# Kernel tuning notes

Hardware: AMD Instinct MI355X
Metric: run time of the kernel (lower is better)

The kernel has to match this reference:

```python
import jax, jax.numpy as jnp
import numpy as np

TEMP = 1.0
PRIOR = 0.2
THRESHOLD = 0.5
EPS = 1.1920929e-07  # torch float32 eps used by probs_to_logits / clamp_probs


def setup_inputs() -> dict:
    key = jax.random.key(0)
    k1, k2, k3, k4, k5 = jax.random.split(key, 5)
    B, L, D = 8, 8192, 256
    hidden = jax.random.normal(k1, (B, L, D), dtype=jnp.float32)
    # q/k projections are initialized to identity in the module; perturb slightly
    Wq = jnp.eye(D, dtype=jnp.float32) + 0.02 * jax.random.normal(k2, (D, D), dtype=jnp.float32)
    Wk = jnp.eye(D, dtype=jnp.float32) + 0.02 * jax.random.normal(k3, (D, D), dtype=jnp.float32)
    # uniform noise for the RelaxedBernoulli reparameterized sample
    noise = jax.random.uniform(k4, (B, L), dtype=jnp.float32)
    # ragged lengths -> contiguous attention mask (1s then 0s), as the module assumes
    lengths = jax.random.randint(k5, (B,), L // 2, L + 1)
    attention_mask = (jnp.arange(L)[None, :] < lengths[:, None]).astype(jnp.float32)
    return {"hidden": hidden, "Wq": Wq, "Wk": Wk, "noise": noise, "attention_mask": attention_mask}


def _binomial_loss(k, n, p):
    # -log Binomial(n, p).log_prob(k) / n
    logp = (jax.scipy.special.gammaln(n + 1.0)
            - jax.scipy.special.gammaln(k + 1.0)
            - jax.scipy.special.gammaln(n - k + 1.0)
            + k * jnp.log(p) + (n - k) * jnp.log1p(-p))
    return -logp / n


def reference(hidden, Wq, Wk, noise, attention_mask):
    B, L, D = hidden.shape
    # F.normalize along last dim (eps=1e-12), then linear projections (no bias)
    hn = hidden / jnp.maximum(jnp.linalg.norm(hidden, axis=-1, keepdims=True), 1e-12)
    q = jnp.einsum('bld,ed->ble', hn[:, :-1], Wq)
    k = jnp.einsum('bld,ed->ble', hn[:, 1:], Wk)
    cos_sim = jnp.sum(q * k, axis=-1)                      # [B, L-1]
    probs = jnp.clip((1.0 - cos_sim) * 0.5, 0.0, 1.0)
    probs = jnp.pad(probs, ((0, 0), (1, 0)), constant_values=1.0)  # boundary forced at t=0

    # RelaxedBernoulli(temp, probs).rsample() with externally supplied uniforms
    p = jnp.clip(probs, EPS, 1.0 - EPS)
    logits = jnp.log(p) - jnp.log1p(-p)
    u = jnp.clip(noise, EPS, 1.0 - EPS)
    soft = jax.nn.sigmoid((logits + jnp.log(u) - jnp.log1p(-u)) / TEMP)
    hard = (soft > THRESHOLD).astype(soft.dtype)
    hard = jax.lax.stop_gradient(hard - soft) + soft       # straight-through

    # mask out boundaries in padding; force a boundary at the last real token
    hard = hard * attention_mask
    pad_mask = attention_mask == 0
    first_pad = pad_mask & (jnp.cumsum(pad_mask.astype(jnp.int32), axis=1) == 1)
    last_real = jnp.roll(first_pad, shift=-1, axis=1).at[:, -1].set(False)
    hard = jnp.maximum(hard, last_real.astype(hard.dtype))

    # downsample: mean-pool tokens within each boundary-delimited segment.
    # boundary==1 starts a new segment; segment id = cumsum(hard) - 1.
    hard_bin = jax.lax.stop_gradient(hard) > 0.5
    seg = jnp.cumsum(hard_bin.astype(jnp.int32), axis=1) - 1
    seg = jnp.clip(seg, 0, L - 1)
    flat_seg = (seg + jnp.arange(B, dtype=jnp.int32)[:, None] * L).reshape(-1)  # [B*L]
    w = attention_mask.reshape(-1)                                              # pads excluded
    sums = jax.ops.segment_sum(hidden.reshape(-1, D) * w[:, None], flat_seg, num_segments=B * L)
    cnts = jax.ops.segment_sum(w, flat_seg, num_segments=B * L)
    pooled = (sums / (cnts + 1e-9)[:, None]).reshape(B, L, D)  # [B, S_max<=L, D], zero-padded

    n_b = jnp.sum(hard, axis=1)                  # boundaries per batch row
    num_boundaries = jnp.sum(n_b)
    total_positions = jnp.sum(attention_mask)
    # gathered mask values at kept positions are all 1 -> prefix-ones of length n_b
    shortened_attention_mask = (jnp.arange(L)[None, :]
                                < jax.lax.stop_gradient(n_b)[:, None]).astype(jnp.float32)
    loss = _binomial_loss(num_boundaries, total_positions, PRIOR)
    return pooled, loss, num_boundaries, total_positions, shortened_attention_mask
```

## Files before the change

kernel.cpp:

```cpp
#include <hip/hip_runtime.h>
#include <hip/hip_bf16.h>
#include <math.h>

#define L_SEQ 8192
#define B_BATCH 8
#define D_DIM 256
#define BL (B_BATCH * L_SEQ)
#define EPS_F 1.1920929e-07f

typedef __attribute__((ext_vector_type(8))) short short8;
typedef __attribute__((ext_vector_type(4))) float f32x4;
typedef __attribute__((ext_vector_type(4))) unsigned short u16x4;


__device__ inline unsigned short f2bf(float x) {
    __hip_bfloat16 b = __float2bfloat16(x);
    return *(unsigned short*)&b;
}
__device__ inline float bf2f(unsigned short u) {
    __hip_bfloat16 b = *(__hip_bfloat16*)&u;
    return __bfloat162float(b);
}

__global__ __launch_bounds__(256) void k_matMpack(
    const float* __restrict__ Wq, const float* __restrict__ Wk,
    unsigned short* __restrict__ Bpack) {
    __shared__ float Aq[64][33];
    __shared__ float Ak[64][17];
    const int f   = blockIdx.x;
    const int k8  = f >> 4, ct = f & 15;
    const int tid = threadIdx.x;
    const int n   = tid & 15;
    const int k   = tid >> 4;
    float a0 = 0.f, a1 = 0.f;
    for (int e0 = 0; e0 < 256; e0 += 64) {
        for (int i = tid; i < 64 * 32; i += 256) {
            const int e = i >> 5, d = i & 31;
            Aq[e][d] = Wq[(e0 + e) * 256 + k8 * 32 + d];
        }
        for (int i = tid; i < 64 * 16; i += 256) {
            const int e = i >> 4, d = i & 15;
            Ak[e][d] = Wk[(e0 + e) * 256 + ct * 16 + d];
        }
        __syncthreads();
#pragma unroll 8
        for (int e = 0; e < 64; ++e) {
            a0 += Aq[e][k] * Ak[e][n];
            a1 += Aq[e][k + 16] * Ak[e][n];
        }
        __syncthreads();
    }
    const int col = ct * 16 + n;
    const float M0 = a0 - ((k8 * 32 + k)      == col ? 1.0f : 0.0f);
    const float M1 = a1 - ((k8 * 32 + k + 16) == col ? 1.0f : 0.0f);
    const unsigned short h0 = f2bf(M0), h1 = f2bf(M1);
    const unsigned short l0 = f2bf(M0 - bf2f(h0)), l1 = f2bf(M1 - bf2f(h1));
    unsigned short* dstH = Bpack + (size_t)(k8 * 16 + ct) * 512;
    unsigned short* dstL = dstH + 128 * 512;
    const int q0 = k >> 3, j0 = k & 7;
    const int q1 = (k + 16) >> 3;
    dstH[(q0 * 16 + n) * 8 + j0] = h0;
    dstH[(q1 * 16 + n) * 8 + j0] = h1;
    dstL[(q0 * 16 + n) * 8 + j0] = l0;
    dstL[(q1 * 16 + n) * 8 + j0] = l1;
}

#define RS 264
#define MM(A,Bv,C) __builtin_amdgcn_mfma_f32_16x16x32_bf16((A),(Bv),(C),0,0,0)
#define MFMA8(V0,V1,BN) \
    acc[0][0]=MM(V0,BN##_0,acc[0][0]); acc[0][1]=MM(V0,BN##_1,acc[0][1]); \
    acc[0][2]=MM(V0,BN##_2,acc[0][2]); acc[0][3]=MM(V0,BN##_3,acc[0][3]); \
    acc[1][0]=MM(V1,BN##_0,acc[1][0]); acc[1][1]=MM(V1,BN##_1,acc[1][1]); \
    acc[1][2]=MM(V1,BN##_2,acc[1][2]); acc[1][3]=MM(V1,BN##_3,acc[1][3]);
#define LOADB(BN,S) \
    BN##_0 = Bld[(((S) * 16) + wc4 + 0) * 64]; \
    BN##_1 = Bld[(((S) * 16) + wc4 + 1) * 64]; \
    BN##_2 = Bld[(((S) * 16) + wc4 + 2) * 64]; \
    BN##_3 = Bld[(((S) * 16) + wc4 + 3) * 64];
#define STRIP_HL(S,BN) { \
    const int co = ((S) & 7) * 32; \
    const short8 hv0 = *(const short8*)(hA0 + co), hv1 = *(const short8*)(hA1 + co); \
    const short8 lv0 = *(const short8*)(lA0 + co), lv1 = *(const short8*)(lA1 + co); \
    MFMA8(hv0, hv1, BN); \
    MFMA8(lv0, lv1, BN); \
    LOADB(BN, (S) + 3); }
#define STRIP_H(S,BN) { \
    const int co = ((S) & 7) * 32; \
    const short8 hv0 = *(const short8*)(hA0 + co), hv1 = *(const short8*)(hA1 + co); \
    MFMA8(hv0, hv1, BN); \
    if ((S) + 3 < 16) { LOADB(BN, (S) + 3); } }

__global__ __launch_bounds__(512, 4) void k_cosmfma(
    const float* __restrict__ hidden, const unsigned short* __restrict__ Bpack,
    const float* __restrict__ noise, unsigned char* __restrict__ hard) {
    __shared__ __attribute__((aligned(16))) unsigned short hiA[65 * RS];
    __shared__ __attribute__((aligned(16))) unsigned short loA[65 * RS];
    __shared__ float Vpart[4][64];
    __shared__ float dots[64];

    const int tid  = threadIdx.x;
    const int lane = tid & 63;
    const int w    = tid >> 6;
    const int wr   = w >> 2;
    const int wc   = w & 3;
    const int wr32 = wr * 32;
    const int wc4  = wc * 4;
    const int T0   = blockIdx.x * 64;

    const short8* __restrict__ Bld = (const short8*)Bpack + lane;

    short8 bA_0, bA_1, bA_2, bA_3, bB_0, bB_1, bB_2, bB_3, bC_0, bC_1, bC_2, bC_3;
    LOADB(bA, 0);
    LOADB(bB, 1);
    LOADB(bC, 2);

    {
        const int r0 = w * 8;
        int tokA = T0 - 1 + r0; if (tokA < 0) tokA = 0;
        float4 vb0 = ((const float4*)hidden)[(size_t)tokA * 64 + lane];
        float4 vb1 = ((const float4*)hidden)[(size_t)(T0 + r0) * 64 + lane];
        float4 hp4 = {0.f, 0.f, 0.f, 0.f};
#pragma unroll 1
        for (int ii = 0; ii <= 8; ++ii) {
            const float4 vcur = vb0;
            vb0 = vb1;
            if (ii + 2 <= 8)
                vb1 = ((const float4*)hidden)[(size_t)(T0 + r0 + ii + 1) * 64 + lane];
            float ss = vcur.x * vcur.x + vcur.y * vcur.y + vcur.z * vcur.z + vcur.w * vcur.w;
#pragma unroll
            for (int sh = 32; sh >= 1; sh >>= 1) ss += __shfl_xor(ss, sh);
            const float inv = 1.0f / fmaxf(sqrtf(ss), 1e-12f);
            float4 h4;
            h4.x = vcur.x * inv; h4.y = vcur.y * inv;
            h4.z = vcur.z * inv; h4.w = vcur.w * inv;
            const unsigned short hx = f2bf(h4.x), hy = f2bf(h4.y),
                                 hz = f2bf(h4.z), hw2 = f2bf(h4.w);
            const u16x4 hv4 = {hx, hy, hz, hw2};
            const u16x4 lv4 = {f2bf(h4.x - bf2f(hx)), f2bf(h4.y - bf2f(hy)),
                               f2bf(h4.z - bf2f(hz)), f2bf(h4.w - bf2f(hw2))};
            const int i = r0 + ii;
            *(u16x4*)&hiA[i * RS + lane * 4] = hv4;
            *(u16x4*)&loA[i * RS + lane * 4] = lv4;
            if (ii > 0) {
                float pd = h4.x * hp4.x + h4.y * hp4.y + h4.z * hp4.z + h4.w * hp4.w;
#pragma unroll
                for (int sh = 32; sh >= 1; sh >>= 1) pd += __shfl_xor(pd, sh);
                if (lane == 0) dots[i - 1] = pd;
            }
            hp4 = h4;
        }
    }
    __syncthreads();

    const int m = lane & 15, q = lane >> 4;
    const unsigned short* __restrict__ hA0 = &hiA[(wr32 +  0 + m) * RS + q * 8];
    const unsigned short* __restrict__ hA1 = &hiA[(wr32 + 16 + m) * RS + q * 8];
    const unsigned short* __restrict__ lA0 = &loA[(wr32 +  0 + m) * RS + q * 8];
    const unsigned short* __restrict__ lA1 = &loA[(wr32 + 16 + m) * RS + q * 8];

    f32x4 acc[2][4];
#pragma unroll
    for (int af = 0; af < 2; ++af)
#pragma unroll
        for (int c = 0; c < 4; ++c) { f32x4 z = {0.f, 0.f, 0.f, 0.f}; acc[af][c] = z; }

    STRIP_HL(0, bA)  STRIP_HL(1, bB)  STRIP_HL(2, bC)  STRIP_HL(3, bA)
    STRIP_HL(4, bB)  STRIP_HL(5, bC)  STRIP_HL(6, bA)  STRIP_HL(7, bB)
    STRIP_H (8, bC)  STRIP_H (9, bA)  STRIP_H (10, bB) STRIP_H (11, bC)
    STRIP_H (12, bA) STRIP_H (13, bB) STRIP_H (14, bC) STRIP_H (15, bA)

#pragma unroll
    for (int af = 0; af < 2; ++af) {
#pragma unroll
        for (int r = 0; r < 4; ++r) {
            const int row = wr32 + af * 16 + (q << 2) + r;
            const int ib  = (row + 1) * RS + wc4 * 16 + m;
            float pp = acc[af][0][r] * (bf2f(hiA[ib     ]) + bf2f(loA[ib     ]))
                     + acc[af][1][r] * (bf2f(hiA[ib + 16]) + bf2f(loA[ib + 16]))
                     + acc[af][2][r] * (bf2f(hiA[ib + 32]) + bf2f(loA[ib + 32]))
                     + acc[af][3][r] * (bf2f(hiA[ib + 48]) + bf2f(loA[ib + 48]));
            pp += __shfl_xor(pp, 1);
            pp += __shfl_xor(pp, 2);
            pp += __shfl_xor(pp, 4);
            pp += __shfl_xor(pp, 8);
            if (m == 0) Vpart[wc][row] = pp;
        }
    }
    __syncthreads();
    if (tid < 64) {
        const int rl = tid;
        const float part = Vpart[0][rl] + Vpart[1][rl] + Vpart[2][rl] + Vpart[3][rl];
        const int t = T0 + rl;
        const int l = t & (L_SEQ - 1);
        float p;
        if (l == 0) {
            p = 1.0f;
        } else {
            p = (1.0f - (part + dots[rl])) * 0.5f;
            p = fminf(fmaxf(p, 0.0f), 1.0f);
        }
        p = fminf(fmaxf(p, EPS_F), 1.0f - EPS_F);
        float u = noise[t];
        u = fminf(fmaxf(u, EPS_F), 1.0f - EPS_F);
        const float z = ((logf(p) - log1pf(-p)) + logf(u)) - log1pf(-u);
        hard[t] = (z > 0.0f) ? (unsigned char)1 : (unsigned char)0;
    }
}

__global__ __launch_bounds__(1024) void k_scan(
    const float* __restrict__ mask, const unsigned char* __restrict__ hard,
    int* __restrict__ starts, int* __restrict__ nb_arr,
    int* __restrict__ len_arr, float* __restrict__ out_short) {
    __shared__ int wsum[16];
    __shared__ int s_len;
    const int b = blockIdx.x, tid = threadIdx.x;
    const int lane = tid & 63, wv = tid >> 6;
    const int base = b * L_SEQ;

    const float4* m4 = (const float4*)(mask + base);
    const float4 va = m4[tid * 2], vb = m4[tid * 2 + 1];
    int cnt = (va.x != 0.f) + (va.y != 0.f) + (va.z != 0.f) + (va.w != 0.f)
            + (vb.x != 0.f) + (vb.y != 0.f) + (vb.z != 0.f) + (vb.w != 0.f);
#pragma unroll
    for (int sh = 32; sh >= 1; sh >>= 1) cnt += __shfl_xor(cnt, sh);
    if (lane == 0) wsum[wv] = cnt;
    __syncthreads();
    if (tid == 0) {
        int s = 0;
        for (int i = 0; i < 16; ++i) s += wsum[i];
        s_len = s;
    }
    __syncthreads();
    const int len = s_len;

    const int i0 = tid * 8;
    const uint2 hb = ((const uint2*)(hard + base))[tid];
    int c = 0;
    unsigned int bits = 0;
#pragma unroll
    for (int j = 0; j < 8; ++j) {
        const unsigned int byte = ((j < 4 ? hb.x : hb.y) >> (8 * (j & 3))) & 0xffu;
        int h = ((i0 + j) < len) ? (int)(byte != 0u) : 0;
        if (len < L_SEQ && (i0 + j) == len - 1) h = 1;
        bits |= (unsigned int)h << j;
        c += h;
    }
    int x = c;
#pragma unroll
    for (int ofs = 1; ofs < 64; ofs <<= 1) {
        const int t = __shfl_up(x, ofs);
        if (lane >= ofs) x += t;
    }
    if (lane == 63) wsum[wv] = x;
    __syncthreads();
    int woff = 0, nb = 0;
#pragma unroll
    for (int i = 0; i < 16; ++i) {
        const int t = wsum[i];
        nb += t;
        if (i < wv) woff += t;
    }
    int run = woff + x - c;
#pragma unroll
    for (int j = 0; j < 8; ++j)
        if ((bits >> j) & 1u) { starts[base + run] = i0 + j; ++run; }

    if (tid == 0) { nb_arr[b] = nb; len_arr[b] = len; }

    float4 o0, o1;
    o0.x = (i0 + 0) < nb ? 1.f : 0.f; o0.y = (i0 + 1) < nb ? 1.f : 0.f;
    o0.z = (i0 + 2) < nb ? 1.f : 0.f; o0.w = (i0 + 3) < nb ? 1.f : 0.f;
    o1.x = (i0 + 4) < nb ? 1.f : 0.f; o1.y = (i0 + 5) < nb ? 1.f : 0.f;
    o1.z = (i0 + 6) < nb ? 1.f : 0.f; o1.w = (i0 + 7) < nb ? 1.f : 0.f;
    float4* os4 = (float4*)(out_short + base);
    os4[tid * 2] = o0;
    os4[tid * 2 + 1] = o1;
}

__global__ __launch_bounds__(256) void k_pool(
    const float* __restrict__ hidden, const int* __restrict__ starts,
    const int* __restrict__ nb_arr, const int* __restrict__ len_arr,
    float* __restrict__ pooled) {
    const int tid  = threadIdx.x;
    const int lane = tid & 63;
    const int wid  = blockIdx.x * 4 + (tid >> 6);
    const int b    = wid >> 13;
    const int s    = wid & (L_SEQ - 1);
    const int nb   = nb_arr[b];

    float4 res = {0.f, 0.f, 0.f, 0.f};
    if (s < nb) {
        const int start = (s == 0) ? 0 : starts[b * L_SEQ + s];
        const int end   = (s + 1 < nb) ? starts[b * L_SEQ + s + 1] : len_arr[b];
        float4 acc = {0.f, 0.f, 0.f, 0.f};
        for (int t = start; t < end; ++t) {
            const float4 v = ((const float4*)hidden)[(b * L_SEQ + t) * 64 + lane];
            acc.x += v.x; acc.y += v.y; acc.z += v.z; acc.w += v.w;
        }
        const float cntf = (float)(end - start);
        res.x = acc.x / cntf; res.y = acc.y / cntf; res.z = acc.z / cntf; res.w = acc.w / cntf;
    }
    ((float4*)pooled)[(size_t)wid * 64 + lane] = res;
}

__global__ void k_final(const int* __restrict__ nb_arr, const int* __restrict__ len_arr,
                        float* __restrict__ out_scal) {
    if (threadIdx.x == 0) {
        int nb = 0, ln = 0;
        for (int b = 0; b < B_BATCH; ++b) { nb += nb_arr[b]; ln += len_arr[b]; }
        const double k = (double)nb, n = (double)ln;
        const double logp = lgamma(n + 1.0) - lgamma(k + 1.0) - lgamma(n - k + 1.0)
                            + k * log(0.2) + (n - k) * log(0.8);
        const double loss = -logp / n;
        out_scal[0] = (float)loss;
        out_scal[1] = (float)nb;
        out_scal[2] = (float)ln;
    }
}

extern "C" void kernel_launch(void* const* d_in, const int* in_sizes, int n_in,
                              void* d_out, int out_size, void* d_ws, size_t ws_size,
                              hipStream_t stream) {
    const float* hidden = (const float*)d_in[0];
    const float* Wq     = (const float*)d_in[1];
    const float* Wk     = (const float*)d_in[2];
    const float* noise  = (const float*)d_in[3];
    const float* mask   = (const float*)d_in[4];
    float* out = (float*)d_out;
    char* ws = (char*)d_ws;

    int*            starts = (int*)(ws);
    unsigned short* Bpack  = (unsigned short*)(ws + 262144);
    unsigned char*  hard   = (unsigned char*)(ws + 524288);
    int*            nb_arr = (int*)(ws + 589824);
    int*            len_arr= (int*)(ws + 589856);

    float* pooled = out;
    float* scal   = out + (size_t)BL * D_DIM;
    float* shortm = scal + 3;

    k_matMpack<<<128, 256, 0, stream>>>(Wq, Wk, Bpack);
    k_cosmfma <<<BL / 64, 512, 0, stream>>>(hidden, Bpack, noise, hard);
    k_scan    <<<B_BATCH, 1024, 0, stream>>>(mask, hard, starts, nb_arr, len_arr, shortm);
    k_pool    <<<BL / 4, 256, 0, stream>>>(hidden, starts, nb_arr, len_arr, pooled);
    k_final   <<<1, 64, 0, stream>>>(nb_arr, len_arr, scal);
}
```

Before: 180.6 us.

## Split MFMA K-dimension across wave pairs instead of splitting rows

Changes the wave decomposition of the cosine-similarity MFMA from splitting the 64 rows across two wave groups to splitting the K dimension in half. Each wave now covers all 64 rows with 4x4 accumulators, and the partial results are reduced across 8 Vpart slots. Each wave now loads only half of the B matrix fragments, which cuts global B traffic and register prefetch depth. In exchange it doubles accumulator registers and adds a larger final reduction, and the occupancy hint moves to an amdgpu_waves_per_eu attribute.

```diff
diff --git a/kernel.cpp b/kernel.cpp
--- a/kernel.cpp
+++ b/kernel.cpp
@@ -67,52 +67,59 @@
 
 #define RS 264
 #define MM(A,Bv,C) __builtin_amdgcn_mfma_f32_16x16x32_bf16((A),(Bv),(C),0,0,0)
-#define MFMA8(V0,V1,BN) \
+#define MFMA16(V0,V1,V2,V3,BN) \
     acc[0][0]=MM(V0,BN##_0,acc[0][0]); acc[0][1]=MM(V0,BN##_1,acc[0][1]); \
     acc[0][2]=MM(V0,BN##_2,acc[0][2]); acc[0][3]=MM(V0,BN##_3,acc[0][3]); \
     acc[1][0]=MM(V1,BN##_0,acc[1][0]); acc[1][1]=MM(V1,BN##_1,acc[1][1]); \
-    acc[1][2]=MM(V1,BN##_2,acc[1][2]); acc[1][3]=MM(V1,BN##_3,acc[1][3]);
-#define LOADB(BN,S) \
-    BN##_0 = Bld[(((S) * 16) + wc4 + 0) * 64]; \
-    BN##_1 = Bld[(((S) * 16) + wc4 + 1) * 64]; \
-    BN##_2 = Bld[(((S) * 16) + wc4 + 2) * 64]; \
-    BN##_3 = Bld[(((S) * 16) + wc4 + 3) * 64];
-#define STRIP_HL(S,BN) { \
-    const int co = ((S) & 7) * 32; \
-    const short8 hv0 = *(const short8*)(hA0 + co), hv1 = *(const short8*)(hA1 + co); \
-    const short8 lv0 = *(const short8*)(lA0 + co), lv1 = *(const short8*)(lA1 + co); \
-    MFMA8(hv0, hv1, BN); \
-    MFMA8(lv0, lv1, BN); \
-    LOADB(BN, (S) + 3); }
-#define STRIP_H(S,BN) { \
-    const int co = ((S) & 7) * 32; \
-    const short8 hv0 = *(const short8*)(hA0 + co), hv1 = *(const short8*)(hA1 + co); \
-    MFMA8(hv0, hv1, BN); \
-    if ((S) + 3 < 16) { LOADB(BN, (S) + 3); } }
-
-__global__ __launch_bounds__(512, 4) void k_cosmfma(
+    acc[1][2]=MM(V1,BN##_2,acc[1][2]); acc[1][3]=MM(V1,BN##_3,acc[1][3]); \
+    acc[2][0]=MM(V2,BN##_0,acc[2][0]); acc[2][1]=MM(V2,BN##_1,acc[2][1]); \
+    acc[2][2]=MM(V2,BN##_2,acc[2][2]); acc[2][3]=MM(V2,BN##_3,acc[2][3]); \
+    acc[3][0]=MM(V3,BN##_0,acc[3][0]); acc[3][1]=MM(V3,BN##_1,acc[3][1]); \
+    acc[3][2]=MM(V3,BN##_2,acc[3][2]); acc[3][3]=MM(V3,BN##_3,acc[3][3]);
+#define LOADB(BN,J) { \
+    BN##_0 = Bw[(((J) < 4 ? (J) : (J) + 4) * 16 + 0) * 64]; \
+    BN##_1 = Bw[(((J) < 4 ? (J) : (J) + 4) * 16 + 1) * 64]; \
+    BN##_2 = Bw[(((J) < 4 ? (J) : (J) + 4) * 16 + 2) * 64]; \
+    BN##_3 = Bw[(((J) < 4 ? (J) : (J) + 4) * 16 + 3) * 64]; }
+#define COMP_HL(J,BN) { \
+    const short8 hv0 = *(const short8*)(hbase2 + ( 0*16)*RS + ((J)&3)*32); \
+    const short8 hv1 = *(const short8*)(hbase2 + ( 1*16)*RS + ((J)&3)*32); \
+    const short8 hv2 = *(const short8*)(hbase2 + ( 2*16)*RS + ((J)&3)*32); \
+    const short8 hv3 = *(const short8*)(hbase2 + ( 3*16)*RS + ((J)&3)*32); \
+    MFMA16(hv0, hv1, hv2, hv3, BN); \
+    const short8 lv0 = *(const short8*)(lbase2 + ( 0*16)*RS + ((J)&3)*32); \
+    const short8 lv1 = *(const short8*)(lbase2 + ( 1*16)*RS + ((J)&3)*32); \
+    const short8 lv2 = *(const short8*)(lbase2 + ( 2*16)*RS + ((J)&3)*32); \
+    const short8 lv3 = *(const short8*)(lbase2 + ( 3*16)*RS + ((J)&3)*32); \
+    MFMA16(lv0, lv1, lv2, lv3, BN); }
+#define COMP_H(J,BN) { \
+    const short8 hv0 = *(const short8*)(hbase2 + ( 0*16)*RS + ((J)&3)*32); \
+    const short8 hv1 = *(const short8*)(hbase2 + ( 1*16)*RS + ((J)&3)*32); \
+    const short8 hv2 = *(const short8*)(hbase2 + ( 2*16)*RS + ((J)&3)*32); \
+    const short8 hv3 = *(const short8*)(hbase2 + ( 3*16)*RS + ((J)&3)*32); \
+    MFMA16(hv0, hv1, hv2, hv3, BN); }
+
+__global__ __launch_bounds__(512) __attribute__((amdgpu_waves_per_eu(4, 4)))
+void k_cosmfma(
     const float* __restrict__ hidden, const unsigned short* __restrict__ Bpack,
     const float* __restrict__ noise, unsigned char* __restrict__ hard) {
     __shared__ __attribute__((aligned(16))) unsigned short hiA[65 * RS];
     __shared__ __attribute__((aligned(16))) unsigned short loA[65 * RS];
-    __shared__ float Vpart[4][64];
+    __shared__ float Vpart[8][64];
     __shared__ float dots[64];
 
     const int tid  = threadIdx.x;
     const int lane = tid & 63;
     const int w    = tid >> 6;
-    const int wr   = w >> 2;
+    const int wk   = w >> 2;
     const int wc   = w & 3;
-    const int wr32 = wr * 32;
     const int wc4  = wc * 4;
     const int T0   = blockIdx.x * 64;
 
-    const short8* __restrict__ Bld = (const short8*)Bpack + lane;
-
-    short8 bA_0, bA_1, bA_2, bA_3, bB_0, bB_1, bB_2, bB_3, bC_0, bC_1, bC_2, bC_3;
+    const short8* __restrict__ Bw = (const short8*)Bpack + ((wk * 4) * 16 + wc4) * 64 + lane;
+
+    short8 bA_0, bA_1, bA_2, bA_3, bB_0, bB_1, bB_2, bB_3;
     LOADB(bA, 0);
-    LOADB(bB, 1);
-    LOADB(bC, 2);
 
     {
         const int r0 = w * 8;
@@ -153,27 +160,29 @@
     __syncthreads();
 
     const int m = lane & 15, q = lane >> 4;
-    const unsigned short* __restrict__ hA0 = &hiA[(wr32 +  0 + m) * RS + q * 8];
-    const unsigned short* __restrict__ hA1 = &hiA[(wr32 + 16 + m) * RS + q * 8];
-    const unsigned short* __restrict__ lA0 = &loA[(wr32 +  0 + m) * RS + q * 8];
-    const unsigned short* __restrict__ lA1 = &loA[(wr32 + 16 + m) * RS + q * 8];
-
-    f32x4 acc[2][4];
-#pragma unroll
-    for (int af = 0; af < 2; ++af)
+    const unsigned short* __restrict__ hbase2 = &hiA[m * RS + q * 8 + wk * 128];
+    const unsigned short* __restrict__ lbase2 = &loA[m * RS + q * 8 + wk * 128];
+
+    f32x4 acc[4][4];
+#pragma unroll
+    for (int af = 0; af < 4; ++af)
 #pragma unroll
         for (int c = 0; c < 4; ++c) { f32x4 z = {0.f, 0.f, 0.f, 0.f}; acc[af][c] = z; }
 
-    STRIP_HL(0, bA)  STRIP_HL(1, bB)  STRIP_HL(2, bC)  STRIP_HL(3, bA)
-    STRIP_HL(4, bB)  STRIP_HL(5, bC)  STRIP_HL(6, bA)  STRIP_HL(7, bB)
-    STRIP_H (8, bC)  STRIP_H (9, bA)  STRIP_H (10, bB) STRIP_H (11, bC)
-    STRIP_H (12, bA) STRIP_H (13, bB) STRIP_H (14, bC) STRIP_H (15, bA)
-
-#pragma unroll
-    for (int af = 0; af < 2; ++af) {
+    LOADB(bB, 1) COMP_HL(0, bA)
+    LOADB(bA, 2) COMP_HL(1, bB)
+    LOADB(bB, 3) COMP_HL(2, bA)
+    LOADB(bA, 4) COMP_HL(3, bB)
+    LOADB(bB, 5) COMP_H (4, bA)
+    LOADB(bA, 6) COMP_H (5, bB)
+    LOADB(bB, 7) COMP_H (6, bA)
+    COMP_H (7, bB)
+
+#pragma unroll
+    for (int af = 0; af < 4; ++af) {
 #pragma unroll
         for (int r = 0; r < 4; ++r) {
-            const int row = wr32 + af * 16 + (q << 2) + r;
+            const int row = af * 16 + (q << 2) + r;
             const int ib  = (row + 1) * RS + wc4 * 16 + m;
             float pp = acc[af][0][r] * (bf2f(hiA[ib     ]) + bf2f(loA[ib     ]))
                      + acc[af][1][r] * (bf2f(hiA[ib + 16]) + bf2f(loA[ib + 16]))
@@ -183,13 +192,14 @@
             pp += __shfl_xor(pp, 2);
             pp += __shfl_xor(pp, 4);
             pp += __shfl_xor(pp, 8);
-            if (m == 0) Vpart[wc][row] = pp;
+            if (m == 0) Vpart[w][row] = pp;
         }
     }
     __syncthreads();
     if (tid < 64) {
         const int rl = tid;
-        const float part = Vpart[0][rl] + Vpart[1][rl] + Vpart[2][rl] + Vpart[3][rl];
+        const float part = Vpart[0][rl] + Vpart[1][rl] + Vpart[2][rl] + Vpart[3][rl]
+                         + Vpart[4][rl] + Vpart[5][rl] + Vpart[6][rl] + Vpart[7][rl];
         const int t = T0 + rl;
         const int l = t & (L_SEQ - 1);
         float p;
```

Result: slower. 226.3 us (+25.3%).
